# Performance work log

Measured on AMD Instinct MI355X. Metric: run time of the kernel, lower is better.

## Reference

```python
import jax, jax.numpy as jnp
import numpy as np

B, S, IN_DIM, D, H, L = 2, 2048, 64, 512, 8, 2
DK = D // H
EPS = 1e-5

def _layernorm(x, g, b):
    mu = jnp.mean(x, axis=-1, keepdims=True)
    var = jnp.mean((x - mu) ** 2, axis=-1, keepdims=True)
    return (x - mu) * jax.lax.rsqrt(var + EPS) * g + b

def _prob_sparse_layer(x, Wq, bq, Wk, bk, Wv, bv, fcW, fcb, ln_g, ln_b):
    # x: [B, S, D]
    Bs, Ss, _ = x.shape
    Q = (x @ Wq + bq).reshape(Bs, Ss, H, DK).transpose(0, 2, 1, 3)  # [B,H,S,DK]
    K = (x @ Wk + bk).reshape(Bs, Ss, H, DK).transpose(0, 2, 1, 3)
    V = (x @ Wv + bv).reshape(Bs, Ss, H, DK).transpose(0, 2, 1, 3)
    scores = jnp.einsum('bhqd,bhkd->bhqk', Q, K) / np.sqrt(DK).astype(np.float32)
    k = max(1, Ss // 10)
    top_scores, _ = jax.lax.top_k(scores, k)          # [B,H,S,k]
    threshold = top_scores[..., -1:]                  # k-th largest per row
    sparse_scores = jnp.where(scores < threshold, -jnp.inf, scores)
    attn = jax.nn.softmax(sparse_scores, axis=-1)     # dropout is identity in eval
    out = jnp.einsum('bhqk,bhkd->bhqd', attn, V)
    out = out.transpose(0, 2, 1, 3).reshape(Bs, Ss, D)
    out = out @ fcW + fcb
    return _layernorm(x + out, ln_g, ln_b)

def setup_inputs() -> dict:
    key = jax.random.key(0)
    ks = jax.random.split(key, 16)
    sd = 1.0 / np.sqrt(D)
    sdi = 1.0 / np.sqrt(IN_DIM)
    return {
        'x': jax.random.normal(ks[0], (B, S, IN_DIM), jnp.float32),
        'enc_W': jax.random.normal(ks[1], (IN_DIM, D), jnp.float32) * sdi,
        'enc_b': jnp.zeros((D,), jnp.float32),
        'Wq': jax.random.normal(ks[2], (L, D, D), jnp.float32) * sd,
        'bq': jnp.zeros((L, D), jnp.float32),
        'Wk': jax.random.normal(ks[3], (L, D, D), jnp.float32) * sd,
        'bk': jnp.zeros((L, D), jnp.float32),
        'Wv': jax.random.normal(ks[4], (L, D, D), jnp.float32) * sd,
        'bv': jnp.zeros((L, D), jnp.float32),
        'fcW': jax.random.normal(ks[5], (L, D, D), jnp.float32) * sd,
        'fcb': jnp.zeros((L, D), jnp.float32),
        'ln_g': jnp.ones((L, D), jnp.float32),
        'ln_b': jnp.zeros((L, D), jnp.float32),
        'dec_W': jax.random.normal(ks[6], (D, IN_DIM), jnp.float32) * sd,
        'dec_b': jnp.zeros((IN_DIM,), jnp.float32),
    }

def reference(x, enc_W, enc_b, Wq, bq, Wk, bk, Wv, bv, fcW, fcb, ln_g, ln_b, dec_W, dec_b):
    h = x @ enc_W + enc_b  # [B,S,D]
    for i in range(Wq.shape[0]):
        h = _prob_sparse_layer(h, Wq[i], bq[i], Wk[i], bk[i], Wv[i], bv[i],
                               fcW[i], fcb[i], ln_g[i], ln_b[i])
    return h[:, -1, :] @ dec_W + dec_b  # [B, IN_DIM]
```

## Files before the change

kernel.cpp:

```cpp
#include <hip/hip_runtime.h>
#include <hip/hip_bf16.h>

typedef unsigned short u16;
typedef __bf16 bf16x8 __attribute__((ext_vector_type(8)));
typedef u16 u16x8 __attribute__((ext_vector_type(8)));
typedef float f32x4 __attribute__((ext_vector_type(4)));

#define S_LEN 2048
#define NH 8
#define DMODEL 512
#define TOPK 204

__device__ __forceinline__ u16 f2b(float f) {
  __hip_bfloat16 h = __float2bfloat16(f);
  return __builtin_bit_cast(u16, h);
}
__device__ __forceinline__ unsigned f2b_fast(float f) {
  unsigned u = __float_as_uint(f);
  return (u + 0x7FFFu + ((u >> 16) & 1u)) >> 16;
}
__device__ __forceinline__ float kunmap(unsigned k) {
  unsigned tb = (k & 0x8000u) ? (k ^ 0x8000u) : (~k & 0xFFFFu);
  return __uint_as_float(tb << 16);
}
__device__ __forceinline__ unsigned fkmap(float f) {
  unsigned b = __float_as_uint(f) >> 16;
  return b ^ ((b & 0x8000u) ? 0xFFFFu : 0x8000u);
}
__device__ __forceinline__ void gload_lds16(const u16* g, u16* l) {
  __builtin_amdgcn_global_load_lds(
      (const __attribute__((address_space(1))) unsigned int*)(unsigned long long)(uintptr_t)g,
      (__attribute__((address_space(3))) unsigned int*)(unsigned)(uintptr_t)l, 16, 0, 0);
}

__global__ void transpose_w(const float* __restrict__ in, u16* __restrict__ out, int R, int C) {
  __shared__ float tile[32][33];
  int c0 = blockIdx.x * 32, r0 = blockIdx.y * 32;
  int tx = threadIdx.x & 31, ty = threadIdx.x >> 5;
#pragma unroll
  for (int i = 0; i < 32; i += 8)
    tile[ty + i][tx] = in[(long long)(r0 + ty + i) * C + c0 + tx];
  __syncthreads();
#pragma unroll
  for (int i = 0; i < 32; i += 8)
    out[(long long)(c0 + ty + i) * R + r0 + tx] = f2b(tile[tx][ty + i]);
}

__global__ void transpose_w4(const float* __restrict__ W0, const float* __restrict__ W1,
                             const float* __restrict__ W2, const float* __restrict__ W3,
                             u16* __restrict__ O0, u16* __restrict__ O1,
                             u16* __restrict__ O2, u16* __restrict__ O3) {
  __shared__ float tile[32][33];
  const float* in;
  u16* out;
  switch (blockIdx.z) {
    case 0: in = W0; out = O0; break;
    case 1: in = W1; out = O1; break;
    case 2: in = W2; out = O2; break;
    default: in = W3; out = O3; break;
  }
  int c0 = blockIdx.x * 32, r0 = blockIdx.y * 32;
  int tx = threadIdx.x & 31, ty = threadIdx.x >> 5;
#pragma unroll
  for (int i = 0; i < 32; i += 8)
    tile[ty + i][tx] = in[(long long)(r0 + ty + i) * 512 + c0 + tx];
  __syncthreads();
#pragma unroll
  for (int i = 0; i < 32; i += 8)
    out[(long long)(c0 + ty + i) * 512 + r0 + tx] = f2b(tile[tx][ty + i]);
}

__global__ void conv_b(const float* __restrict__ in, u16* __restrict__ out, int n) {
  int i = blockIdx.x * 256 + threadIdx.x;
  if (i < n) out[i] = f2b(in[i]);
}

template <int MODE>
__global__ __launch_bounds__(256) void gemm_bt(
    const u16* __restrict__ A, const u16* __restrict__ BT,
    const float* __restrict__ bias, const float* __restrict__ biasK, const float* __restrict__ biasV,
    float* __restrict__ outF, u16* __restrict__ outB, u16* __restrict__ outBK, u16* __restrict__ outBV,
    int M, int N, int K, float scale) {
  __shared__ u16 As[64 * 32];
  __shared__ u16 Bs[128 * 32];
  int n0 = blockIdx.x * 128, m0 = blockIdx.y * 64;
  int t = threadIdx.x;
  int lane = t & 63, wv = t >> 6;
  int mw = (wv & 1) * 32, nw = (wv >> 1) * 64;
  int fr = lane & 15, fg = lane >> 4;
  int e0 = t * 8;
  int r0r = e0 >> 5, c0c = e0 & 31;
  int e1 = e0 + 2048;
  int r1r = e1 >> 5, c1c = e1 & 31;
  f32x4 acc[2][4] = {};
  for (int kt = 0; kt < K; kt += 32) {
    gload_lds16(&A[(long long)(m0 + r0r) * K + kt + c0c], &As[e0]);
    gload_lds16(&BT[(long long)(n0 + r0r) * K + kt + c0c], &Bs[e0]);
    gload_lds16(&BT[(long long)(n0 + r1r) * K + kt + c1c], &Bs[e1]);
    __syncthreads();
    bf16x8 af[2], bfv[4];
#pragma unroll
    for (int i = 0; i < 2; i++) af[i] = *(const bf16x8*)&As[(mw + i * 16 + fr) * 32 + fg * 8];
#pragma unroll
    for (int j = 0; j < 4; j++) bfv[j] = *(const bf16x8*)&Bs[(nw + j * 16 + fr) * 32 + fg * 8];
#pragma unroll
    for (int i = 0; i < 2; i++)
#pragma unroll
      for (int j = 0; j < 4; j++)
        acc[i][j] = __builtin_amdgcn_mfma_f32_16x16x32_bf16(af[i], bfv[j], acc[i][j], 0, 0, 0);
    __syncthreads();
  }
#pragma unroll
  for (int i = 0; i < 2; i++)
#pragma unroll
    for (int j = 0; j < 4; j++) {
      int mloc = mw + i * 16 + fg * 4;
      int n = n0 + nw + j * 16 + fr;
      float bvl;
      if constexpr (MODE == 5) {
        int seg = n >> 9, nn = n & 511;
        bvl = (seg == 0 ? bias : seg == 1 ? biasK : biasV)[nn];
      } else {
        bvl = bias ? bias[n] : 0.f;
      }
#pragma unroll
      for (int r = 0; r < 4; r++) {
        int m = m0 + mloc + r;
        float v = acc[i][j][r] * scale + bvl;
        if constexpr (MODE == 0) {
          outF[(long long)m * N + n] = v;
        } else if constexpr (MODE == 4) {
          outF[(long long)m * N + n] = v;
          outB[(long long)m * N + n] = f2b(v);
        } else if constexpr (MODE == 5) {
          int seg = n >> 9, nn = n & 511;
          if (seg == 0) v *= 0.125f;
          u16 val = f2b(v);
          if (seg == 2) {
            outBV[((long long)((m >> 11) * NH + (nn >> 6)) * 64 + (nn & 63)) * S_LEN + (m & 2047)] = val;
          } else {
            long long qkidx = (long long)((m >> 11) * NH + (nn >> 6)) * (S_LEN * 64) +
                              (long long)(m & 2047) * 64 + (nn & 63);
            if (seg == 0) outB[qkidx] = val;
            else outBK[qkidx] = val;
          }
        }
      }
    }
}

__global__ __launch_bounds__(1024, 8) void score_pv(
    const u16* __restrict__ Qb, const u16* __restrict__ Kb, const u16* __restrict__ VTb,
    u16* __restrict__ aoB) {
  __shared__ u16 Qs[16 * 64];
  __shared__ __align__(16) u16 Ss[16 * 2048];
  __shared__ float thrS[16];
  __shared__ float mS[16];
  __shared__ float zS[16 * 16];
  int flat = blockIdx.x;
  int xcd = flat & 7, local = flat >> 3;
  int bh = xcd * 2 + (local >> 7);
  int m0 = (local & 127) * 16;
  int t = threadIdx.x;
  int lane = t & 63, wv = t >> 6, fr = lane & 15, fg = lane >> 4;
  const u16* Qg = Qb + ((long long)bh * S_LEN + m0) * 64;
  const u16* Kg = Kb + (long long)bh * S_LEN * 64;
  const u16* Vg = VTb + (long long)bh * 64 * S_LEN;
  if (t < 128) {
    int row = t >> 3, cc = t & 7;
    *(u16x8*)&Qs[row * 64 + ((cc ^ (row & 7)) * 8)] = *(const u16x8*)&Qg[row * 64 + cc * 8];
  }
  __syncthreads();
  bf16x8 aq[2];
#pragma unroll
  for (int ks = 0; ks < 2; ks++)
    aq[ks] = *(const bf16x8*)&Qs[fr * 64 + (((fg + 4 * ks) ^ (fr & 7)) * 8)];

  int colb = wv * 128;
  unsigned sw = (unsigned)((fr & 15) << 3);
  unsigned sbase = (unsigned)(fr * 2048);
  const u16* kp = Kg + (long long)(colb + fr) * 64 + fg * 8;
#pragma unroll
  for (int tt = 0; tt < 8; tt++) {
    bf16x8 bk0 = *(const bf16x8*)(kp);
    bf16x8 bk1 = *(const bf16x8*)(kp + 32);
    f32x4 acc = {};
    __builtin_amdgcn_s_setprio(1);
    acc = __builtin_amdgcn_mfma_f32_16x16x32_bf16(bk0, aq[0], acc, 0, 0, 0);
    acc = __builtin_amdgcn_mfma_f32_16x16x32_bf16(bk1, aq[1], acc, 0, 0, 0);
    __builtin_amdgcn_s_setprio(0);
    uint2 w;
    w.x = f2b_fast(acc[0]) | (f2b_fast(acc[1]) << 16);
    w.y = f2b_fast(acc[2]) | (f2b_fast(acc[3]) << 16);
    unsigned col = (unsigned)(colb + tt * 16 + fg * 4);
    *(uint2*)&Ss[sbase + (col ^ sw)] = w;
    kp += 16 * 64;
  }
  __syncthreads();

  {
    int rr = wv;
    const uint2* cu2 = (const uint2*)&Ss[rr * 2048];
    float kf[32];
#pragma unroll
    for (int j = 0; j < 8; j++) {
      uint2 w = cu2[lane + 64 * j];
      kf[4 * j + 0] = __uint_as_float(w.x << 16);
      kf[4 * j + 1] = __uint_as_float(w.x & 0xFFFF0000u);
      kf[4 * j + 2] = __uint_as_float(w.y << 16);
      kf[4 * j + 3] = __uint_as_float(w.y & 0xFFFF0000u);
    }
    float mxf = kf[0];
#pragma unroll
    for (int j = 1; j < 32; j++) mxf = fmaxf(mxf, kf[j]);
#pragma unroll
    for (int o = 1; o < 64; o <<= 1)
      mxf = fmaxf(mxf, __uint_as_float((unsigned)__shfl_xor((int)__float_as_uint(mxf), o)));
    unsigned mxi = fkmap(mxf);
    unsigned lo, hi;
    if (mxi > 384u) {
      unsigned lo0 = mxi - 384u;
      float pf = kunmap(lo0);
      int c = 0;
#pragma unroll
      for (int j = 0; j < 32; j++) c += (int)__popcll(__ballot(kf[j] >= pf));
      if (c >= TOPK) { lo = lo0; hi = mxi; }
      else { lo = 0u; hi = lo0 - 1u; }
    } else {
      lo = 0u; hi = mxi;
    }
    while (lo < hi) {
      unsigned mid = (lo + hi + 1u) >> 1;
      float midf = kunmap(mid);
      int c = 0;
#pragma unroll
      for (int j = 0; j < 32; j++) c += (int)__popcll(__ballot(kf[j] >= midf));
      if (c >= TOPK) lo = mid; else hi = mid - 1u;
    }
    if (lane == 0) {
      thrS[rr] = kunmap(lo);
      mS[rr] = mxf;
    }
  }
  __syncthreads();

  float thrF = thrS[fr];
  float myM = mS[fr];
  float zpart = 0.f;
  f32x4 acc_o[4] = {};
  int kbase = wv * 128;
  const u16* vp0 = Vg + (long long)fr * 2048 + kbase + fg * 8;
  const u16* vp1 = vp0 + 16 * 2048;
  const u16* vp2 = vp1 + 16 * 2048;
  const u16* vp3 = vp2 + 16 * 2048;
#pragma unroll
  for (int step = 0; step < 4; step++) {
    int k0 = kbase + step * 32;
    u16x8 kk = *(const u16x8*)&Ss[sbase + (((unsigned)(k0 + fg * 8)) ^ sw)];
    unsigned wp[4];
#pragma unroll
    for (int e2 = 0; e2 < 4; e2++) {
      float s0 = __uint_as_float((unsigned)kk[2 * e2] << 16);
      float s1 = __uint_as_float((unsigned)kk[2 * e2 + 1] << 16);
      float p0 = (s0 >= thrF) ? __expf(s0 - myM) : 0.f;
      float p1 = (s1 >= thrF) ? __expf(s1 - myM) : 0.f;
      zpart += p0 + p1;
      wp[e2] = f2b_fast(p0) | (f2b_fast(p1) << 16);
    }
    bf16x8 pa = *(bf16x8*)&wp;
    bf16x8 bv0 = *(const bf16x8*)(vp0 + step * 32);
    bf16x8 bv1 = *(const bf16x8*)(vp1 + step * 32);
    bf16x8 bv2 = *(const bf16x8*)(vp2 + step * 32);
    bf16x8 bv3 = *(const bf16x8*)(vp3 + step * 32);
    __builtin_amdgcn_s_setprio(1);
    acc_o[0] = __builtin_amdgcn_mfma_f32_16x16x32_bf16(pa, bv0, acc_o[0], 0, 0, 0);
    acc_o[1] = __builtin_amdgcn_mfma_f32_16x16x32_bf16(pa, bv1, acc_o[1], 0, 0, 0);
    acc_o[2] = __builtin_amdgcn_mfma_f32_16x16x32_bf16(pa, bv2, acc_o[2], 0, 0, 0);
    acc_o[3] = __builtin_amdgcn_mfma_f32_16x16x32_bf16(pa, bv3, acc_o[3], 0, 0, 0);
    __builtin_amdgcn_s_setprio(0);
  }
  zpart += __shfl_xor(zpart, 16);
  zpart += __shfl_xor(zpart, 32);
  __syncthreads();

  float* Of = (float*)Ss;
#pragma unroll
  for (int j = 0; j < 4; j++)
#pragma unroll
    for (int r = 0; r < 4; r++) {
      int row = fg * 4 + r, col = j * 16 + fr;
      Of[wv * 1024 + row * 64 + (col ^ ((row >> 2) << 3))] = acc_o[j][r];
    }
  if (fg == 0) zS[wv * 16 + fr] = zpart;
  __syncthreads();
  long long ob = (long long)(bh >> 3) * S_LEN * DMODEL + (bh & 7) * 64;
  {
    int row = t >> 6, dk = t & 63;
    int sw2 = dk ^ ((row >> 2) << 3);
    float s = 0.f;
#pragma unroll
    for (int w = 0; w < 16; w++) s += Of[w * 1024 + row * 64 + sw2];
    float z = 0.f;
#pragma unroll
    for (int w = 0; w < 16; w++) z += zS[w * 16 + row];
    aoB[ob + (long long)(m0 + row) * DMODEL + dk] = f2b(s / z);
  }
}

__global__ __launch_bounds__(256) void resid_ln(const float* __restrict__ h, const float* __restrict__ fco,
                                                const float* __restrict__ g, const float* __restrict__ b,
                                                float* __restrict__ hout, u16* __restrict__ hbout) {
  __shared__ float red[4];
  int row = blockIdx.x;
  int t = threadIdx.x;
  long long base = (long long)row * 512;
  float v0 = h[base + t] + fco[base + t];
  float v1 = h[base + t + 256] + fco[base + t + 256];
  float s = v0 + v1;
#pragma unroll
  for (int o = 32; o > 0; o >>= 1) s += __shfl_down(s, o);
  if ((t & 63) == 0) red[t >> 6] = s;
  __syncthreads();
  float mu = (red[0] + red[1] + red[2] + red[3]) * (1.f / 512.f);
  float d0 = v0 - mu, d1 = v1 - mu;
  float q = d0 * d0 + d1 * d1;
#pragma unroll
  for (int o = 32; o > 0; o >>= 1) q += __shfl_down(q, o);
  __syncthreads();
  if ((t & 63) == 0) red[t >> 6] = q;
  __syncthreads();
  float var = (red[0] + red[1] + red[2] + red[3]) * (1.f / 512.f);
  float rs = rsqrtf(var + 1e-5f);
  float y0 = d0 * rs * g[t] + b[t];
  float y1 = d1 * rs * g[t + 256] + b[t + 256];
  hout[base + t] = y0;
  hout[base + t + 256] = y1;
  hbout[base + t] = f2b(y0);
  hbout[base + t + 256] = f2b(y1);
}

__global__ __launch_bounds__(512) void decoder_k(const float* __restrict__ h, const float* __restrict__ W,
                                                 const float* __restrict__ bias, float* __restrict__ out) {
  __shared__ float part[8][64];
  int b = blockIdx.x;
  int t = threadIdx.x;
  int j = t & 63, ds = t >> 6;
  const float* hr = h + ((long long)b * S_LEN + (S_LEN - 1)) * DMODEL;
  float s = 0.f;
#pragma unroll 8
  for (int d = ds * 64; d < ds * 64 + 64; d++) s += hr[d] * W[(long long)d * 64 + j];
  part[ds][j] = s;
  __syncthreads();
  if (t < 64) {
    float acc = part[0][t];
#pragma unroll
    for (int w = 1; w < 8; w++) acc += part[w][t];
    out[b * 64 + t] = acc + bias[t];
  }
}

extern "C" void kernel_launch(void* const* d_in, const int* in_sizes, int n_in,
                              void* d_out, int out_size, void* d_ws, size_t ws_size,
                              hipStream_t stream) {
  const float* x = (const float*)d_in[0];
  const float* enc_W = (const float*)d_in[1];
  const float* enc_b = (const float*)d_in[2];
  const float* Wq = (const float*)d_in[3];
  const float* bq = (const float*)d_in[4];
  const float* Wk = (const float*)d_in[5];
  const float* bk = (const float*)d_in[6];
  const float* Wv = (const float*)d_in[7];
  const float* bv = (const float*)d_in[8];
  const float* fcW = (const float*)d_in[9];
  const float* fcb = (const float*)d_in[10];
  const float* ln_g = (const float*)d_in[11];
  const float* ln_b = (const float*)d_in[12];
  const float* dec_W = (const float*)d_in[13];
  const float* dec_b = (const float*)d_in[14];

  char* p = (char*)d_ws;
  auto alloc = [&](size_t bytes) {
    char* r = p;
    p += (bytes + 255) & ~(size_t)255;
    return r;
  };
  const size_t BS = 2 * (size_t)S_LEN;
  u16* encWT = (u16*)alloc(512 * 64 * 2);
  u16* xbf = (u16*)alloc(BS * 64 * 2);
  float* hF = (float*)alloc(BS * 512 * 4);
  u16* hB = (u16*)alloc(BS * 512 * 2);
  u16* WqT = (u16*)alloc(512 * 512 * 2);
  u16* WkT = (u16*)alloc(512 * 512 * 2);
  u16* WvT = (u16*)alloc(512 * 512 * 2);
  u16* fcWT = (u16*)alloc(512 * 512 * 2);
  u16* Qb = (u16*)alloc((size_t)16 * 2048 * 64 * 2);
  u16* Kb = (u16*)alloc((size_t)16 * 2048 * 64 * 2);
  u16* VTb = (u16*)alloc((size_t)16 * 2048 * 64 * 2);
  u16* aoB = (u16*)alloc(BS * 512 * 2);
  float* fcO = (float*)Qb;

  transpose_w<<<dim3(16, 2), 256, 0, stream>>>(enc_W, encWT, 64, 512);
  conv_b<<<(int)(BS * 64 / 256), 256, 0, stream>>>(x, xbf, (int)(BS * 64));
  gemm_bt<4><<<dim3(4, 64), 256, 0, stream>>>(xbf, encWT, enc_b, nullptr, nullptr,
                                              hF, hB, nullptr, nullptr, 4096, 512, 64, 1.f);

  for (int l = 0; l < 2; l++) {
    transpose_w4<<<dim3(16, 16, 4), 256, 0, stream>>>(
        Wq + (size_t)l * 512 * 512, Wk + (size_t)l * 512 * 512,
        Wv + (size_t)l * 512 * 512, fcW + (size_t)l * 512 * 512,
        WqT, WkT, WvT, fcWT);
    gemm_bt<5><<<dim3(12, 64), 256, 0, stream>>>(hB, WqT, bq + l * 512, bk + l * 512, bv + l * 512,
                                                 nullptr, Qb, Kb, VTb, 4096, 1536, 512, 1.f);
    score_pv<<<dim3(2048), 1024, 0, stream>>>(Qb, Kb, VTb, aoB);
    gemm_bt<0><<<dim3(4, 64), 256, 0, stream>>>(aoB, fcWT, fcb + l * 512, nullptr, nullptr,
                                                fcO, nullptr, nullptr, nullptr, 4096, 512, 512, 1.f);
    resid_ln<<<4096, 256, 0, stream>>>(hF, fcO, ln_g + l * 512, ln_b + l * 512, hF, hB);
  }
  decoder_k<<<2, 512, 0, stream>>>(hF, dec_W, dec_b, (float*)d_out);
}
```

Before: 363.6 us.

## Process 32 query rows per score_pv block to reuse K and V loads

Each score_pv block now handles 32 query rows instead of 16, with two row groups sharing every K fragment in the score MFMAs and every V fragment in the PV MFMAs. The grid halves and per-thread work doubles, including two top-k threshold searches per wave. This cuts global K/V traffic per query row, at the cost of doubled shared memory (about 128KB for scores), more registers, and lower occupancy (launch bounds lowered to 4).

```diff
diff --git a/kernel.cpp b/kernel.cpp
--- a/kernel.cpp
+++ b/kernel.cpp
@@ -149,57 +149,66 @@
     }
 }
 
-__global__ __launch_bounds__(1024, 8) void score_pv(
+__global__ __launch_bounds__(1024, 4) void score_pv(
     const u16* __restrict__ Qb, const u16* __restrict__ Kb, const u16* __restrict__ VTb,
     u16* __restrict__ aoB) {
-  __shared__ u16 Qs[16 * 64];
-  __shared__ __align__(16) u16 Ss[16 * 2048];
-  __shared__ float thrS[16];
-  __shared__ float mS[16];
-  __shared__ float zS[16 * 16];
+  __shared__ u16 Qs[32 * 64];
+  __shared__ __align__(16) u16 Ss[32 * 2048];
+  __shared__ float thrS[32];
+  __shared__ float mS[32];
+  __shared__ float zS[16 * 32];
   int flat = blockIdx.x;
   int xcd = flat & 7, local = flat >> 3;
-  int bh = xcd * 2 + (local >> 7);
-  int m0 = (local & 127) * 16;
+  int bh = xcd * 2 + (local >> 6);
+  int m0 = (local & 63) * 32;
   int t = threadIdx.x;
   int lane = t & 63, wv = t >> 6, fr = lane & 15, fg = lane >> 4;
   const u16* Qg = Qb + ((long long)bh * S_LEN + m0) * 64;
   const u16* Kg = Kb + (long long)bh * S_LEN * 64;
   const u16* Vg = VTb + (long long)bh * 64 * S_LEN;
-  if (t < 128) {
+  if (t < 256) {
     int row = t >> 3, cc = t & 7;
-    *(u16x8*)&Qs[row * 64 + ((cc ^ (row & 7)) * 8)] = *(const u16x8*)&Qg[row * 64 + cc * 8];
-  }
-  __syncthreads();
-  bf16x8 aq[2];
-#pragma unroll
-  for (int ks = 0; ks < 2; ks++)
-    aq[ks] = *(const bf16x8*)&Qs[fr * 64 + (((fg + 4 * ks) ^ (fr & 7)) * 8)];
+    *(u16x8*)&Qs[row * 64 + ((cc ^ (row & 7)) * 8)] = *(const u16x8*)&Qg[(long long)row * 64 + cc * 8];
+  }
+  __syncthreads();
+  bf16x8 aqA[2], aqB[2];
+#pragma unroll
+  for (int ks = 0; ks < 2; ks++) {
+    aqA[ks] = *(const bf16x8*)&Qs[fr * 64 + (((fg + 4 * ks) ^ (fr & 7)) * 8)];
+    aqB[ks] = *(const bf16x8*)&Qs[(fr + 16) * 64 + (((fg + 4 * ks) ^ (fr & 7)) * 8)];
+  }
 
   int colb = wv * 128;
   unsigned sw = (unsigned)((fr & 15) << 3);
-  unsigned sbase = (unsigned)(fr * 2048);
+  unsigned sbaseA = (unsigned)(fr * 2048);
+  unsigned sbaseB = (unsigned)((fr + 16) * 2048);
   const u16* kp = Kg + (long long)(colb + fr) * 64 + fg * 8;
 #pragma unroll
   for (int tt = 0; tt < 8; tt++) {
     bf16x8 bk0 = *(const bf16x8*)(kp);
     bf16x8 bk1 = *(const bf16x8*)(kp + 32);
-    f32x4 acc = {};
+    f32x4 accA = {}, accB = {};
     __builtin_amdgcn_s_setprio(1);
-    acc = __builtin_amdgcn_mfma_f32_16x16x32_bf16(bk0, aq[0], acc, 0, 0, 0);
-    acc = __builtin_amdgcn_mfma_f32_16x16x32_bf16(bk1, aq[1], acc, 0, 0, 0);
+    accA = __builtin_amdgcn_mfma_f32_16x16x32_bf16(bk0, aqA[0], accA, 0, 0, 0);
+    accA = __builtin_amdgcn_mfma_f32_16x16x32_bf16(bk1, aqA[1], accA, 0, 0, 0);
+    accB = __builtin_amdgcn_mfma_f32_16x16x32_bf16(bk0, aqB[0], accB, 0, 0, 0);
+    accB = __builtin_amdgcn_mfma_f32_16x16x32_bf16(bk1, aqB[1], accB, 0, 0, 0);
     __builtin_amdgcn_s_setprio(0);
-    uint2 w;
-    w.x = f2b_fast(acc[0]) | (f2b_fast(acc[1]) << 16);
-    w.y = f2b_fast(acc[2]) | (f2b_fast(acc[3]) << 16);
     unsigned col = (unsigned)(colb + tt * 16 + fg * 4);
-    *(uint2*)&Ss[sbase + (col ^ sw)] = w;
+    uint2 wA, wB;
+    wA.x = f2b_fast(accA[0]) | (f2b_fast(accA[1]) << 16);
+    wA.y = f2b_fast(accA[2]) | (f2b_fast(accA[3]) << 16);
+    wB.x = f2b_fast(accB[0]) | (f2b_fast(accB[1]) << 16);
+    wB.y = f2b_fast(accB[2]) | (f2b_fast(accB[3]) << 16);
+    *(uint2*)&Ss[sbaseA + (col ^ sw)] = wA;
+    *(uint2*)&Ss[sbaseB + (col ^ sw)] = wB;
     kp += 16 * 64;
   }
   __syncthreads();
 
-  {
-    int rr = wv;
+#pragma unroll
+  for (int g = 0; g < 2; g++) {
+    int rr = wv + g * 16;
     const uint2* cu2 = (const uint2*)&Ss[rr * 2048];
     float kf[32];
 #pragma unroll
@@ -244,10 +253,10 @@
   }
   __syncthreads();
 
-  float thrF = thrS[fr];
-  float myM = mS[fr];
-  float zpart = 0.f;
-  f32x4 acc_o[4] = {};
+  float thrA = thrS[fr], mA = mS[fr];
+  float thrB = thrS[fr + 16], mB = mS[fr + 16];
+  float zA = 0.f, zB = 0.f;
+  f32x4 accOA[4] = {}, accOB[4] = {};
   int kbase = wv * 128;
   const u16* vp0 = Vg + (long long)fr * 2048 + kbase + fg * 8;
   const u16* vp1 = vp0 + 16 * 2048;
@@ -256,31 +265,46 @@
 #pragma unroll
   for (int step = 0; step < 4; step++) {
     int k0 = kbase + step * 32;
-    u16x8 kk = *(const u16x8*)&Ss[sbase + (((unsigned)(k0 + fg * 8)) ^ sw)];
-    unsigned wp[4];
+    unsigned koff = ((unsigned)(k0 + fg * 8)) ^ sw;
+    u16x8 kkA = *(const u16x8*)&Ss[sbaseA + koff];
+    u16x8 kkB = *(const u16x8*)&Ss[sbaseB + koff];
+    unsigned wpA[4], wpB[4];
 #pragma unroll
     for (int e2 = 0; e2 < 4; e2++) {
-      float s0 = __uint_as_float((unsigned)kk[2 * e2] << 16);
-      float s1 = __uint_as_float((unsigned)kk[2 * e2 + 1] << 16);
-      float p0 = (s0 >= thrF) ? __expf(s0 - myM) : 0.f;
-      float p1 = (s1 >= thrF) ? __expf(s1 - myM) : 0.f;
-      zpart += p0 + p1;
-      wp[e2] = f2b_fast(p0) | (f2b_fast(p1) << 16);
-    }
-    bf16x8 pa = *(bf16x8*)&wp;
+      float sA0 = __uint_as_float((unsigned)kkA[2 * e2] << 16);
+      float sA1 = __uint_as_float((unsigned)kkA[2 * e2 + 1] << 16);
+      float pA0 = (sA0 >= thrA) ? __expf(sA0 - mA) : 0.f;
+      float pA1 = (sA1 >= thrA) ? __expf(sA1 - mA) : 0.f;
+      zA += pA0 + pA1;
+      wpA[e2] = f2b_fast(pA0) | (f2b_fast(pA1) << 16);
+      float sB0 = __uint_as_float((unsigned)kkB[2 * e2] << 16);
+      float sB1 = __uint_as_float((unsigned)kkB[2 * e2 + 1] << 16);
+      float pB0 = (sB0 >= thrB) ? __expf(sB0 - mB) : 0.f;
+      float pB1 = (sB1 >= thrB) ? __expf(sB1 - mB) : 0.f;
+      zB += pB0 + pB1;
+      wpB[e2] = f2b_fast(pB0) | (f2b_fast(pB1) << 16);
+    }
+    bf16x8 paA = *(bf16x8*)&wpA;
+    bf16x8 paB = *(bf16x8*)&wpB;
     bf16x8 bv0 = *(const bf16x8*)(vp0 + step * 32);
     bf16x8 bv1 = *(const bf16x8*)(vp1 + step * 32);
     bf16x8 bv2 = *(const bf16x8*)(vp2 + step * 32);
     bf16x8 bv3 = *(const bf16x8*)(vp3 + step * 32);
     __builtin_amdgcn_s_setprio(1);
-    acc_o[0] = __builtin_amdgcn_mfma_f32_16x16x32_bf16(pa, bv0, acc_o[0], 0, 0, 0);
-    acc_o[1] = __builtin_amdgcn_mfma_f32_16x16x32_bf16(pa, bv1, acc_o[1], 0, 0, 0);
-    acc_o[2] = __builtin_amdgcn_mfma_f32_16x16x32_bf16(pa, bv2, acc_o[2], 0, 0, 0);
-    acc_o[3] = __builtin_amdgcn_mfma_f32_16x16x32_bf16(pa, bv3, acc_o[3], 0, 0, 0);
+    accOA[0] = __builtin_amdgcn_mfma_f32_16x16x32_bf16(paA, bv0, accOA[0], 0, 0, 0);
+    accOA[1] = __builtin_amdgcn_mfma_f32_16x16x32_bf16(paA, bv1, accOA[1], 0, 0, 0);
+    accOA[2] = __builtin_amdgcn_mfma_f32_16x16x32_bf16(paA, bv2, accOA[2], 0, 0, 0);
+    accOA[3] = __builtin_amdgcn_mfma_f32_16x16x32_bf16(paA, bv3, accOA[3], 0, 0, 0);
+    accOB[0] = __builtin_amdgcn_mfma_f32_16x16x32_bf16(paB, bv0, accOB[0], 0, 0, 0);
+    accOB[1] = __builtin_amdgcn_mfma_f32_16x16x32_bf16(paB, bv1, accOB[1], 0, 0, 0);
+    accOB[2] = __builtin_amdgcn_mfma_f32_16x16x32_bf16(paB, bv2, accOB[2], 0, 0, 0);
+    accOB[3] = __builtin_amdgcn_mfma_f32_16x16x32_bf16(paB, bv3, accOB[3], 0, 0, 0);
     __builtin_amdgcn_s_setprio(0);
   }
-  zpart += __shfl_xor(zpart, 16);
-  zpart += __shfl_xor(zpart, 32);
+  zA += __shfl_xor(zA, 16);
+  zA += __shfl_xor(zA, 32);
+  zB += __shfl_xor(zB, 16);
+  zB += __shfl_xor(zB, 32);
   __syncthreads();
 
   float* Of = (float*)Ss;
@@ -288,21 +312,27 @@
   for (int j = 0; j < 4; j++)
 #pragma unroll
     for (int r = 0; r < 4; r++) {
-      int row = fg * 4 + r, col = j * 16 + fr;
-      Of[wv * 1024 + row * 64 + (col ^ ((row >> 2) << 3))] = acc_o[j][r];
-    }
-  if (fg == 0) zS[wv * 16 + fr] = zpart;
+      int rowA = fg * 4 + r, col = j * 16 + fr;
+      Of[wv * 2048 + rowA * 64 + (col ^ ((rowA >> 2) << 3))] = accOA[j][r];
+      int rowB = rowA + 16;
+      Of[wv * 2048 + rowB * 64 + (col ^ ((rowB >> 2) << 3))] = accOB[j][r];
+    }
+  if (fg == 0) {
+    zS[wv * 32 + fr] = zA;
+    zS[wv * 32 + 16 + fr] = zB;
+  }
   __syncthreads();
   long long ob = (long long)(bh >> 3) * S_LEN * DMODEL + (bh & 7) * 64;
-  {
-    int row = t >> 6, dk = t & 63;
+#pragma unroll
+  for (int o = t; o < 2048; o += 1024) {
+    int row = o >> 6, dk = o & 63;
     int sw2 = dk ^ ((row >> 2) << 3);
     float s = 0.f;
 #pragma unroll
-    for (int w = 0; w < 16; w++) s += Of[w * 1024 + row * 64 + sw2];
+    for (int w = 0; w < 16; w++) s += Of[w * 2048 + row * 64 + sw2];
     float z = 0.f;
 #pragma unroll
-    for (int w = 0; w < 16; w++) z += zS[w * 16 + row];
+    for (int w = 0; w < 16; w++) z += zS[w * 32 + row];
     aoB[ob + (long long)(m0 + row) * DMODEL + dk] = f2b(s / z);
   }
 }
@@ -411,7 +441,7 @@
         WqT, WkT, WvT, fcWT);
     gemm_bt<5><<<dim3(12, 64), 256, 0, stream>>>(hB, WqT, bq + l * 512, bk + l * 512, bv + l * 512,
                                                  nullptr, Qb, Kb, VTb, 4096, 1536, 512, 1.f);
-    score_pv<<<dim3(2048), 1024, 0, stream>>>(Qb, Kb, VTb, aoB);
+    score_pv<<<dim3(1024), 1024, 0, stream>>>(Qb, Kb, VTb, aoB);
     gemm_bt<0><<<dim3(4, 64), 256, 0, stream>>>(aoB, fcWT, fcb + l * 512, nullptr, nullptr,
                                                 fcO, nullptr, nullptr, nullptr, 4096, 512, 512, 1.f);
     resid_ln<<<4096, 256, 0, stream>>>(hF, fcO, ln_g + l * 512, ln_b + l * 512, hF, hB);
```

Measured after the change: 366.8 us. No clear change (+0.9%).
